# Performance work log

Measured on AMD Instinct MI355X. Metric: run time of the kernel, lower is better.

The kernel has to match this reference:

```python
import jax, jax.numpy as jnp
import numpy as np

U, P, D, H, E = 512, 1024, 128, 256, 98304
N = U + P


def setup_inputs() -> dict:
    key = jax.random.key(0)
    ks = jax.random.split(key, 16)
    def nrm(k, shape, scale=0.05):
        return jax.random.normal(k, shape, jnp.float32) * scale
    z = lambda *s: jnp.zeros(s, jnp.float32)
    return {
        "user_ids": jnp.arange(U),
        "paper_ids": jnp.arange(P),
        "edge_index": jax.random.randint(ks[0], (2, E), 0, N),
        "user_paper_interactions": jax.random.uniform(ks[1], (U, P), jnp.float32),
        "user_emb": nrm(ks[2], (U, D), 1.0),   # nn.Embedding tables
        "paper_emb": nrm(ks[3], (P, D), 1.0),
        "W0": nrm(ks[4], (D, H)), "b0": z(H),   # GCNConv weights (stored [in,out])
        "W1": nrm(ks[5], (H, H)), "b1": z(H),
        "W2": nrm(ks[6], (H, H)), "b2": z(H),
        "Wu": nrm(ks[7], (H, D)), "bu": z(D),   # user_output Linear
        "Wp": nrm(ks[8], (H, D)), "bp": z(D),   # paper_output Linear
        "Wq1": nrm(ks[9], (2 * D, H)), "bq1": z(H),  # predictor Linear 1
        "Wq2": nrm(ks[10], (H, 1)), "bq2": z(1),      # predictor Linear 2
    }


def gcn_conv(x, src, dst, W, b):
    """PyG GCNConv: add self-loops, symmetric D^-1/2 (A+I) D^-1/2 normalization."""
    n = x.shape[0]
    loop = jnp.arange(n)
    s = jnp.concatenate([src, loop])
    d = jnp.concatenate([dst, loop])
    deg = jax.ops.segment_sum(jnp.ones(d.shape, x.dtype), d, num_segments=n)
    dis = jnp.where(deg > 0, jax.lax.rsqrt(jnp.maximum(deg, 1.0)), 0.0)
    norm = dis[s] * dis[d]                      # [E+n]
    h = x @ W                                   # [n, H]
    out = jax.ops.segment_sum(h[s] * norm[:, None], d, num_segments=n)
    return out + b


def reference(user_ids, paper_ids, edge_index, user_paper_interactions,
              user_emb, paper_emb, W0, b0, W1, b1, W2, b2,
              Wu, bu, Wp, bp, Wq1, bq1, Wq2, bq2):
    # embedding lookups + node feature matrix [U+P, D]
    x = jnp.concatenate([user_emb[user_ids], paper_emb[paper_ids]], axis=0)
    src, dst = edge_index[0], edge_index[1]
    for W, b in ((W0, b0), (W1, b1), (W2, b2)):
        x = jax.nn.relu(gcn_conv(x, src, dst, W, b))  # dropout is identity in eval
    nu = user_ids.shape[0]
    np_ = paper_ids.shape[0]
    user_final = x[:nu] @ Wu + bu               # [U, D]
    paper_final = x[nu:] @ Wp + bp              # [P, D]
    # broadcast outer-product concat -> [U, P, 2D]
    combined = jnp.concatenate([
        jnp.broadcast_to(user_final[:, None, :], (nu, np_, user_final.shape[-1])),
        jnp.broadcast_to(paper_final[None, :, :], (nu, np_, paper_final.shape[-1])),
    ], axis=-1)
    h = jax.nn.relu(combined @ Wq1 + bq1)       # [U, P, H]
    pred = jax.nn.sigmoid(h @ Wq2 + bq2)[..., 0]  # [U, P]
    return pred
```

## Files before the change

### kernel.cpp

```cpp
#include <hip/hip_runtime.h>
#include <math.h>

constexpr int Uc = 512;
constexpr int Pc = 1024;
constexpr int Dc = 128;
constexpr int Hc = 256;
constexpr int Ec = 98304;
constexpr int Nc = 1536;
constexpr int CAP = 192;
constexpr int GRID = 768;
constexpr int BAR_STRIDE = 2304;

__device__ __forceinline__ void st_wt(float* p, float v) {
    __hip_atomic_store(p, v, __ATOMIC_RELAXED, __HIP_MEMORY_SCOPE_AGENT);
}
__device__ __forceinline__ void st_wt_i(int* p, int v) {
    __hip_atomic_store(p, v, __ATOMIC_RELAXED, __HIP_MEMORY_SCOPE_AGENT);
}
__device__ __forceinline__ void st_wt2(float* p, float2 v) {
    unsigned long long u;
    __builtin_memcpy(&u, &v, 8);
    __hip_atomic_store((unsigned long long*)p, u, __ATOMIC_RELAXED,
                       __HIP_MEMORY_SCOPE_AGENT);
}

__device__ __forceinline__ void gbar3(int* bb, int b) {
    __syncthreads();
    if (threadIdx.x == 0) {
        int leaf = b & 63;
        int lc = __hip_atomic_fetch_add(bb + leaf * 16, 1,
                                        __ATOMIC_RELAXED, __HIP_MEMORY_SCOPE_AGENT);
        if (lc == 11) {
            int mc = __hip_atomic_fetch_add(bb + 1024 + (leaf >> 3) * 16, 1,
                                            __ATOMIC_RELAXED, __HIP_MEMORY_SCOPE_AGENT);
            if (mc == 7) {
                int rc = __hip_atomic_fetch_add(bb + 1152, 1,
                                                __ATOMIC_RELAXED, __HIP_MEMORY_SCOPE_AGENT);
                if (rc == 7) {
#pragma unroll
                    for (int i = 0; i < 64; i++)
                        __hip_atomic_store(bb + 1216 + i * 16, 1, __ATOMIC_RELAXED,
                                           __HIP_MEMORY_SCOPE_AGENT);
                }
            }
        }
        int iters = 0;
        while (__hip_atomic_load(bb + 1216 + leaf * 16, __ATOMIC_RELAXED,
                                 __HIP_MEMORY_SCOPE_AGENT) == 0) {
            __builtin_amdgcn_s_sleep(8);
            if (++iters > (1 << 22)) break;
        }
    }
    __syncthreads();
}

__device__ __forceinline__ void fma4(float4& a, float n, const float4 r) {
    a.x += n * r.x; a.y += n * r.y; a.z += n * r.z; a.w += n * r.w;
}

union __align__(16) SharedU {
    struct {
        const float* sptr[2][CAP];
        float snrm[2][CAP];
        float pagg[4][Dc];
        float aggT[Dc][2];
        float red[4][2][Hc];
    } l0;
    struct {
        int sidx[2][CAP];
        float snrm[2][CAP];
        float pagg[4][Hc];
        float aggT[Hc][2];
        float xlocT[Hc][2];
        float red[4][2][Hc];
    } lh;
    struct {
        float auS[Hc * 8];
    } pr;
};

template <int K>
__device__ __forceinline__ void gemm_core16(const float* __restrict__ xr,
                                            const float* __restrict__ wc, int M,
                                            float& acc0, float& acc1) {
#pragma unroll 4
    for (int k = 0; k < K; k += 4) {
        float4 a = *(const float4*)(xr + k);
        float2 b0 = *(const float2*)(wc + (size_t)k * M);
        float2 b1 = *(const float2*)(wc + (size_t)(k + 1) * M);
        float2 b2 = *(const float2*)(wc + (size_t)(k + 2) * M);
        float2 b3 = *(const float2*)(wc + (size_t)(k + 3) * M);
        acc0 += a.x * b0.x; acc1 += a.x * b0.y;
        acc0 += a.y * b1.x; acc1 += a.y * b1.y;
        acc0 += a.z * b2.x; acc1 += a.z * b2.y;
        acc0 += a.w * b3.x; acc1 += a.w * b3.y;
    }
}

__device__ __forceinline__ void phase_front(
        int b, int t,
        const int* __restrict__ e_src, const int* __restrict__ e_dst,
        int* __restrict__ cnt, int* __restrict__ colF,
        const float* __restrict__ Wu, const float* __restrict__ Wp,
        const float* __restrict__ Wq1, const float* __restrict__ bu,
        const float* __restrict__ bp, const float* __restrict__ bq1,
        float* __restrict__ Wup, float* __restrict__ Wpp,
        float* __restrict__ bvu, float* __restrict__ bvp) {
    if (b < 384) {
        int e = b * 256 + t;
        int d = e_dst[e];
        int pos = atomicAdd(&cnt[d], 1);
        if (pos < CAP) st_wt_i(&colF[d * CAP + pos], e_src[e]);
    } else if (b < 640) {
        int id = b - 384;
        int z = id >> 7, tile = id & 127;
        int tx = t & 15, ty = t >> 4;
        const float* X = z ? Wp : Wu;
        const float* W = Wq1 + (z ? (size_t)Dc * Hc : 0);
        float* Y = z ? Wpp : Wup;
        int row = (tile >> 3) * 16 + ty, col = (tile & 7) * 32 + tx * 2;
        float a0 = 0.f, a1 = 0.f;
        gemm_core16<Dc>(X + (size_t)row * Dc, W + col, Hc, a0, a1);
        st_wt2(&Y[(size_t)row * Hc + col], make_float2(a0, a1));
    } else if (b == 640) {
        float s = bq1[t];
#pragma unroll 8
        for (int d = 0; d < Dc; d++) s += bu[d] * Wq1[d * Hc + t];
        st_wt(&bvu[t], s);
    } else if (b == 641) {
        float s = 0.f;
#pragma unroll 8
        for (int d = 0; d < Dc; d++) s += bp[d] * Wq1[(Dc + d) * Hc + t];
        st_wt(&bvp[t], s);
    }
}

__device__ void phase_l0(SharedU& su, int b, int t,
        const int* __restrict__ uid, const int* __restrict__ pid,
        const float* __restrict__ ue, const float* __restrict__ pe,
        const float* __restrict__ W0, const float* __restrict__ b0,
        const int* __restrict__ cnt, const int* __restrict__ colF,
        float* __restrict__ out) {
    int ibase = b * 2;
    int c[2]; float di[2];
#pragma unroll
    for (int r = 0; r < 2; r++) {
        c[r] = cnt[ibase + r];
        di[r] = rsqrtf((float)(c[r] + 1));
        int deg = min(c[r], CAP);
        if (t < deg) {
            int s = colF[(ibase + r) * CAP + t];
            su.l0.sptr[r][t] = (s < Uc) ? ue + (size_t)uid[s] * Dc
                                        : pe + (size_t)pid[s - Uc] * Dc;
            su.l0.snrm[r][t] = rsqrtf((float)(cnt[s] + 1));
        }
    }
    __syncthreads();
    {
        int wv = t >> 6, ln = t & 63;
        int r = wv >> 1, h = wv & 1;
        int i = ibase + r;
        int dg = min(c[r], CAP);
        int dg2 = dg >> 1;
        int j0 = h ? dg2 : 0, j1 = h ? dg : dg2;
        float2 acc = make_float2(0.f, 0.f);
        if (h == 0) {
            const float* xi = (i < Uc) ? ue + (size_t)uid[i] * Dc
                                       : pe + (size_t)pid[i - Uc] * Dc;
            float2 a2 = *(const float2*)(xi + ln * 2);
            acc.x = di[r] * a2.x;
            acc.y = di[r] * a2.y;
        }
        int j = j0;
        for (; j + 8 <= j1; j += 8) {
            float n0 = su.l0.snrm[r][j],     n1 = su.l0.snrm[r][j + 1];
            float n2 = su.l0.snrm[r][j + 2], n3 = su.l0.snrm[r][j + 3];
            float n4 = su.l0.snrm[r][j + 4], n5 = su.l0.snrm[r][j + 5];
            float n6 = su.l0.snrm[r][j + 6], n7 = su.l0.snrm[r][j + 7];
            float2 r0 = *(const float2*)(su.l0.sptr[r][j]     + ln * 2);
            float2 r1 = *(const float2*)(su.l0.sptr[r][j + 1] + ln * 2);
            float2 r2 = *(const float2*)(su.l0.sptr[r][j + 2] + ln * 2);
            float2 r3 = *(const float2*)(su.l0.sptr[r][j + 3] + ln * 2);
            float2 r4 = *(const float2*)(su.l0.sptr[r][j + 4] + ln * 2);
            float2 r5 = *(const float2*)(su.l0.sptr[r][j + 5] + ln * 2);
            float2 r6 = *(const float2*)(su.l0.sptr[r][j + 6] + ln * 2);
            float2 r7 = *(const float2*)(su.l0.sptr[r][j + 7] + ln * 2);
            acc.x += n0 * r0.x + n1 * r1.x + n2 * r2.x + n3 * r3.x;
            acc.y += n0 * r0.y + n1 * r1.y + n2 * r2.y + n3 * r3.y;
            acc.x += n4 * r4.x + n5 * r5.x + n6 * r6.x + n7 * r7.x;
            acc.y += n4 * r4.y + n5 * r5.y + n6 * r6.y + n7 * r7.y;
        }
        for (; j + 4 <= j1; j += 4) {
            float n0 = su.l0.snrm[r][j],     n1 = su.l0.snrm[r][j + 1];
            float n2 = su.l0.snrm[r][j + 2], n3 = su.l0.snrm[r][j + 3];
            float2 r0 = *(const float2*)(su.l0.sptr[r][j]     + ln * 2);
            float2 r1 = *(const float2*)(su.l0.sptr[r][j + 1] + ln * 2);
            float2 r2 = *(const float2*)(su.l0.sptr[r][j + 2] + ln * 2);
            float2 r3 = *(const float2*)(su.l0.sptr[r][j + 3] + ln * 2);
            acc.x += n0 * r0.x + n1 * r1.x + n2 * r2.x + n3 * r3.x;
            acc.y += n0 * r0.y + n1 * r1.y + n2 * r2.y + n3 * r3.y;
        }
        for (; j < j1; j++) {
            float2 r0 = *(const float2*)(su.l0.sptr[r][j] + ln * 2);
            acc.x += su.l0.snrm[r][j] * r0.x;
            acc.y += su.l0.snrm[r][j] * r0.y;
        }
        su.l0.pagg[wv][ln * 2]     = acc.x;
        su.l0.pagg[wv][ln * 2 + 1] = acc.y;
    }
    __syncthreads();
    {
        int r = t >> 7, f = t & 127;
        su.l0.aggT[f][r] = di[r] * (su.l0.pagg[2 * r][f] + su.l0.pagg[2 * r + 1][f]);
    }
    __syncthreads();
    {
        int wv = t >> 6, ln = t & 63;
        int k0 = wv * (Dc / 4);
        float4 a0 = {0.f, 0.f, 0.f, 0.f}, a1 = {0.f, 0.f, 0.f, 0.f};
        const float* Wp_ = W0 + (size_t)k0 * Hc + ln * 4;
#pragma unroll 8
        for (int kk = 0; kk < Dc / 4; kk++) {
            float2 g = *(const float2*)&su.l0.aggT[k0 + kk][0];
            float4 w = *(const float4*)(Wp_ + (size_t)kk * Hc);
            a0.x += g.x * w.x; a0.y += g.x * w.y; a0.z += g.x * w.z; a0.w += g.x * w.w;
            a1.x += g.y * w.x; a1.y += g.y * w.y; a1.z += g.y * w.z; a1.w += g.y * w.w;
        }
        *(float4*)&su.l0.red[wv][0][ln * 4] = a0;
        *(float4*)&su.l0.red[wv][1][ln * 4] = a1;
    }
    __syncthreads();
    {
        float bb = b0[t];
        float s0 = (su.l0.red[0][0][t] + su.l0.red[1][0][t]) +
                   (su.l0.red[2][0][t] + su.l0.red[3][0][t]) + bb;
        float s1 = (su.l0.red[0][1][t] + su.l0.red[1][1][t]) +
                   (su.l0.red[2][1][t] + su.l0.red[3][1][t]) + bb;
        st_wt(&out[(size_t)(ibase + 0) * Hc + t], fmaxf(s0, 0.f));
        st_wt(&out[(size_t)(ibase + 1) * Hc + t], fmaxf(s1, 0.f));
    }
}

__device__ __forceinline__ void agg_wave2(const float* __restrict__ X,
                                          const int (*sidx)[CAP], const float (*snrm)[CAP],
                                          const int* c, const float* di, int ibase,
                                          float (*pagg)[Hc], int t) {
    int wv = t >> 6, ln = t & 63;
    int r = wv >> 1, h = wv & 1;
    int dg = min(c[r], CAP);
    int dg2 = dg >> 1;
    int j0 = h ? dg2 : 0, j1 = h ? dg : dg2;
    float4 acc = make_float4(0.f, 0.f, 0.f, 0.f);
    if (h == 0) {
        acc = *(const float4*)&X[(size_t)(ibase + r) * Hc + ln * 4];
        acc.x *= di[r]; acc.y *= di[r]; acc.z *= di[r]; acc.w *= di[r];
    }
    int j = j0;
    for (; j + 8 <= j1; j += 8) {
        float n0 = snrm[r][j],     n1 = snrm[r][j + 1];
        float n2 = snrm[r][j + 2], n3 = snrm[r][j + 3];
        float n4 = snrm[r][j + 4], n5 = snrm[r][j + 5];
        float n6 = snrm[r][j + 6], n7 = snrm[r][j + 7];
        float4 r0 = *(const float4*)&X[sidx[r][j]     + ln * 4];
        float4 r1 = *(const float4*)&X[sidx[r][j + 1] + ln * 4];
        float4 r2 = *(const float4*)&X[sidx[r][j + 2] + ln * 4];
        float4 r3 = *(const float4*)&X[sidx[r][j + 3] + ln * 4];
        float4 r4 = *(const float4*)&X[sidx[r][j + 4] + ln * 4];
        float4 r5 = *(const float4*)&X[sidx[r][j + 5] + ln * 4];
        float4 r6 = *(const float4*)&X[sidx[r][j + 6] + ln * 4];
        float4 r7 = *(const float4*)&X[sidx[r][j + 7] + ln * 4];
        fma4(acc, n0, r0); fma4(acc, n1, r1); fma4(acc, n2, r2); fma4(acc, n3, r3);
        fma4(acc, n4, r4); fma4(acc, n5, r5); fma4(acc, n6, r6); fma4(acc, n7, r7);
    }
    for (; j + 4 <= j1; j += 4) {
        float n0 = snrm[r][j],     n1 = snrm[r][j + 1];
        float n2 = snrm[r][j + 2], n3 = snrm[r][j + 3];
        float4 r0 = *(const float4*)&X[sidx[r][j]     + ln * 4];
        float4 r1 = *(const float4*)&X[sidx[r][j + 1] + ln * 4];
        float4 r2 = *(const float4*)&X[sidx[r][j + 2] + ln * 4];
        float4 r3 = *(const float4*)&X[sidx[r][j + 3] + ln * 4];
        fma4(acc, n0, r0); fma4(acc, n1, r1); fma4(acc, n2, r2); fma4(acc, n3, r3);
    }
    for (; j < j1; j++) {
        float4 r0 = *(const float4*)&X[sidx[r][j] + ln * 4];
        fma4(acc, snrm[r][j], r0);
    }
    *(float4*)&pagg[wv][ln * 4] = acc;
}

__device__ __forceinline__ void gemv_wsplit(const float (*aggT)[2],
                                            const float* __restrict__ W,
                                            float (*red)[2][Hc], int t) {
    int wv = t >> 6, ln = t & 63;
    int k0 = wv * (Hc / 4);
    float4 a0 = {0.f, 0.f, 0.f, 0.f}, a1 = {0.f, 0.f, 0.f, 0.f};
    const float* Wp_ = W + (size_t)k0 * Hc + ln * 4;
#pragma unroll 8
    for (int kk = 0; kk < Hc / 4; kk++) {
        float2 g = *(const float2*)&aggT[k0 + kk][0];
        float4 w = *(const float4*)(Wp_ + (size_t)kk * Hc);
        a0.x += g.x * w.x; a0.y += g.x * w.y; a0.z += g.x * w.z; a0.w += g.x * w.w;
        a1.x += g.y * w.x; a1.y += g.y * w.y; a1.z += g.y * w.z; a1.w += g.y * w.w;
    }
    *(float4*)&red[wv][0][ln * 4] = a0;
    *(float4*)&red[wv][1][ln * 4] = a1;
}

__device__ __forceinline__ void layer_head(SharedU& su, int b, int t,
        const float* __restrict__ X, const int* __restrict__ cnt,
        const int* __restrict__ colF, int* c, float* di) {
    int ibase = b * 2;
#pragma unroll
    for (int r = 0; r < 2; r++) {
        c[r] = cnt[ibase + r];
        di[r] = rsqrtf((float)(c[r] + 1));
        int deg = min(c[r], CAP);
        if (t < deg) {
            int s = colF[(ibase + r) * CAP + t];
            su.lh.sidx[r][t] = s * Hc;
            su.lh.snrm[r][t] = rsqrtf((float)(cnt[s] + 1));
        }
    }
    __syncthreads();
    agg_wave2(X, su.lh.sidx, su.lh.snrm, c, di, ibase, su.lh.pagg, t);
    __syncthreads();
    *(float2*)&su.lh.aggT[t][0] =
        make_float2(di[0] * (su.lh.pagg[0][t] + su.lh.pagg[1][t]),
                    di[1] * (su.lh.pagg[2][t] + su.lh.pagg[3][t]));
    __syncthreads();
}

__device__ void phase_lh(SharedU& su, int b, int t,
        const float* __restrict__ X, const float* __restrict__ W,
        const float* __restrict__ bias, const int* __restrict__ cnt,
        const int* __restrict__ colF, float* __restrict__ out) {
    int c[2]; float di[2];
    layer_head(su, b, t, X, cnt, colF, c, di);
    gemv_wsplit(su.lh.aggT, W, su.lh.red, t);
    __syncthreads();
    int ibase = b * 2;
    float bb = bias[t];
    float s0 = (su.lh.red[0][0][t] + su.lh.red[1][0][t]) +
               (su.lh.red[2][0][t] + su.lh.red[3][0][t]) + bb;
    float s1 = (su.lh.red[0][1][t] + su.lh.red[1][1][t]) +
               (su.lh.red[2][1][t] + su.lh.red[3][1][t]) + bb;
    st_wt(&out[(size_t)(ibase + 0) * Hc + t], fmaxf(s0, 0.f));
    st_wt(&out[(size_t)(ibase + 1) * Hc + t], fmaxf(s1, 0.f));
}

__device__ void phase_lht(SharedU& su, int b, int t,
        const float* __restrict__ X, const float* __restrict__ W2,
        const float* __restrict__ b2, const int* __restrict__ cnt,
        const int* __restrict__ colF,
        const float* __restrict__ Wup, const float* __restrict__ Wpp,
        const float* __restrict__ bvu, const float* __restrict__ bvp,
        float* __restrict__ AuT, float* __restrict__ ApT) {
    int c[2]; float di[2];
    layer_head(su, b, t, X, cnt, colF, c, di);
    gemv_wsplit(su.lh.aggT, W2, su.lh.red, t);
    __syncthreads();
    {
        float bb = b2[t];
        float s0 = (su.lh.red[0][0][t] + su.lh.red[1][0][t]) +
                   (su.lh.red[2][0][t] + su.lh.red[3][0][t]) + bb;
        float s1 = (su.lh.red[0][1][t] + su.lh.red[1][1][t]) +
                   (su.lh.red[2][1][t] + su.lh.red[3][1][t]) + bb;
        *(float2*)&su.lh.xlocT[t][0] = make_float2(fmaxf(s0, 0.f), fmaxf(s1, 0.f));
    }
    __syncthreads();
    gemv_wsplit(su.lh.xlocT, (b < 256) ? Wup : Wpp, su.lh.red, t);
    __syncthreads();
    {
        int ibase = b * 2;
        const float* bsel = (b < 256) ? bvu : bvp;
        float* YT  = (b < 256) ? AuT : ApT;
        int ldy    = (b < 256) ? Uc : Pc;
        int rloc   = (b < 256) ? ibase : ibase - Uc;
        float bb = bsel[t];
        float s0 = (su.lh.red[0][0][t] + su.lh.red[1][0][t]) +
                   (su.lh.red[2][0][t] + su.lh.red[3][0][t]) + bb;
        float s1 = (su.lh.red[0][1][t] + su.lh.red[1][1][t]) +
                   (su.lh.red[2][1][t] + su.lh.red[3][1][t]) + bb;
        st_wt2(&YT[(size_t)t * ldy + rloc], make_float2(s0, s1));
    }
}

__device__ void phase_pred(float* auS, int b, int t,
        const float* __restrict__ AuT, const float* __restrict__ ApT,
        const float* __restrict__ Wq2, const float* __restrict__ bq2,
        float* __restrict__ out) {
    int ub = (b >> 3) * 8, pb = (b & 7) * 128;
#pragma unroll
    for (int i = t; i < Hc * 8; i += 256) {
        int k = i >> 3, u = i & 7;
        auS[i] = AuT[(size_t)k * Uc + ub + u];
    }
    __syncthreads();
    int wv = t >> 6, ln = t & 63;
    const float* app = ApT + pb + ln * 2;
    const float* aup = auS + wv * 2;
    float acc[2][2] = {};
#pragma unroll 4
    for (int k = 0; k < Hc; k++) {
        float w = Wq2[k];
        float2 a = *(const float2*)(aup + k * 8);
        float2 p = *(const float2*)(app + (size_t)k * Pc);
        acc[0][0] += fmaxf(a.x + p.x, 0.f) * w;
        acc[0][1] += fmaxf(a.x + p.y, 0.f) * w;
        acc[1][0] += fmaxf(a.y + p.x, 0.f) * w;
        acc[1][1] += fmaxf(a.y + p.y, 0.f) * w;
    }
    float bq = bq2[0];
#pragma unroll
    for (int r = 0; r < 2; r++) {
        int u = ub + wv * 2 + r;
        float2 o;
        o.x = 1.f / (1.f + __expf(-(acc[r][0] + bq)));
        o.y = 1.f / (1.f + __expf(-(acc[r][1] + bq)));
        *(float2*)&out[(size_t)u * Pc + pb + ln * 2] = o;
    }
}

struct KArgs {
    const int *uid, *pid, *e_src, *e_dst;
    const float *ue, *pe;
    const float *W0, *b0, *W1, *b1, *W2, *b2;
    const float *Wu, *bu, *Wp, *bp, *Wq1, *bq1, *Wq2, *bq2;
    int *cnt, *colF, *bar;
    float *xA, *xB, *Wup, *Wpp, *bvu, *bvp, *AuT, *ApT, *pred;
};

__global__ void __launch_bounds__(256) k_all(KArgs A) {
    __shared__ SharedU su;
    int t = threadIdx.x, b = blockIdx.x;
    phase_front(b, t, A.e_src, A.e_dst, A.cnt, A.colF, A.Wu, A.Wp, A.Wq1,
                A.bu, A.bp, A.bq1, A.Wup, A.Wpp, A.bvu, A.bvp);
    gbar3(A.bar + 0 * BAR_STRIDE, b);
    phase_l0(su, b, t, A.uid, A.pid, A.ue, A.pe, A.W0, A.b0, A.cnt, A.colF, A.xA);
    gbar3(A.bar + 1 * BAR_STRIDE, b);
    phase_lh(su, b, t, A.xA, A.W1, A.b1, A.cnt, A.colF, A.xB);
    gbar3(A.bar + 2 * BAR_STRIDE, b);
    phase_lht(su, b, t, A.xB, A.W2, A.b2, A.cnt, A.colF,
              A.Wup, A.Wpp, A.bvu, A.bvp, A.AuT, A.ApT);
    gbar3(A.bar + 3 * BAR_STRIDE, b);
    if (b < 512) phase_pred(su.pr.auS, b, t, A.AuT, A.ApT, A.Wq2, A.bq2, A.pred);
}

extern "C" void kernel_launch(void* const* d_in, const int* in_sizes, int n_in,
                              void* d_out, int out_size, void* d_ws, size_t ws_size,
                              hipStream_t stream) {
    KArgs A;
    A.uid = (const int*)d_in[0];
    A.pid = (const int*)d_in[1];
    const int* ei = (const int*)d_in[2];
    A.e_src = ei;
    A.e_dst = ei + Ec;
    A.ue  = (const float*)d_in[4];
    A.pe  = (const float*)d_in[5];
    A.W0  = (const float*)d_in[6];  A.b0  = (const float*)d_in[7];
    A.W1  = (const float*)d_in[8];  A.b1  = (const float*)d_in[9];
    A.W2  = (const float*)d_in[10]; A.b2  = (const float*)d_in[11];
    A.Wu  = (const float*)d_in[12]; A.bu  = (const float*)d_in[13];
    A.Wp  = (const float*)d_in[14]; A.bp  = (const float*)d_in[15];
    A.Wq1 = (const float*)d_in[16]; A.bq1 = (const float*)d_in[17];
    A.Wq2 = (const float*)d_in[18]; A.bq2 = (const float*)d_in[19];

    char* w = (char*)d_ws;
    auto alloc = [&](size_t bytes) { char* p = w; w += (bytes + 255) & ~size_t(255); return p; };
    constexpr int BAR_BYTES = 4 * BAR_STRIDE * 4;
    int* zreg = (int*)alloc(Nc * 4 + BAR_BYTES);
    A.cnt  = zreg;
    A.bar  = zreg + Nc;
    A.colF = (int*)alloc((size_t)Nc * CAP * 4);
    A.xA   = (float*)alloc((size_t)Nc * Hc * 4);
    A.xB   = (float*)alloc((size_t)Nc * Hc * 4);
    A.Wup  = (float*)alloc((size_t)Hc * Hc * 4);
    A.Wpp  = (float*)alloc((size_t)Hc * Hc * 4);
    A.bvu  = (float*)alloc(Hc * 4);
    A.bvp  = (float*)alloc(Hc * 4);
    A.AuT  = (float*)alloc((size_t)Hc * Uc * 4);
    A.ApT  = (float*)alloc((size_t)Hc * Pc * 4);
    A.pred = (float*)d_out;

    hipMemsetAsync(A.cnt, 0, Nc * 4 + BAR_BYTES, stream);
    k_all<<<GRID, 256, 0, stream>>>(A);
}
```

Measured before the change: 193.9 us.

## Replace grid barriers between GCN layers with per-block dataflow flags

```diff
diff --git a/kernel.cpp b/kernel.cpp
--- a/kernel.cpp
+++ b/kernel.cpp
@@ -9,6 +9,7 @@
 constexpr int Nc = 1536;
 constexpr int CAP = 192;
 constexpr int GRID = 768;
+constexpr int CSTR = 16;
 constexpr int BAR_STRIDE = 2304;
 
 __device__ __forceinline__ void st_wt(float* p, float v) {
@@ -22,6 +23,15 @@
     __builtin_memcpy(&u, &v, 8);
     __hip_atomic_store((unsigned long long*)p, u, __ATOMIC_RELAXED,
                        __HIP_MEMORY_SCOPE_AGENT);
+}
+
+__device__ __forceinline__ void wait_ep(const int* ep, int blk) {
+    int it = 0;
+    while (__hip_atomic_load(ep + blk, __ATOMIC_RELAXED,
+                             __HIP_MEMORY_SCOPE_AGENT) == 0) {
+        __builtin_amdgcn_s_sleep(4);
+        if (++it > (1 << 22)) break;
+    }
 }
 
 __device__ __forceinline__ void gbar3(int* bb, int b) {
@@ -109,7 +119,7 @@
     if (b < 384) {
         int e = b * 256 + t;
         int d = e_dst[e];
-        int pos = atomicAdd(&cnt[d], 1);
+        int pos = atomicAdd(&cnt[d * CSTR], 1);
         if (pos < CAP) st_wt_i(&colF[d * CAP + pos], e_src[e]);
     } else if (b < 640) {
         int id = b - 384;
@@ -140,19 +150,19 @@
         const float* __restrict__ ue, const float* __restrict__ pe,
         const float* __restrict__ W0, const float* __restrict__ b0,
         const int* __restrict__ cnt, const int* __restrict__ colF,
-        float* __restrict__ out) {
+        float* __restrict__ out, int* __restrict__ ep1) {
     int ibase = b * 2;
     int c[2]; float di[2];
 #pragma unroll
     for (int r = 0; r < 2; r++) {
-        c[r] = cnt[ibase + r];
+        c[r] = cnt[(ibase + r) * CSTR];
         di[r] = rsqrtf((float)(c[r] + 1));
         int deg = min(c[r], CAP);
         if (t < deg) {
             int s = colF[(ibase + r) * CAP + t];
             su.l0.sptr[r][t] = (s < Uc) ? ue + (size_t)uid[s] * Dc
                                         : pe + (size_t)pid[s - Uc] * Dc;
-            su.l0.snrm[r][t] = rsqrtf((float)(cnt[s] + 1));
+            su.l0.snrm[r][t] = rsqrtf((float)(cnt[s * CSTR] + 1));
         }
     }
     __syncthreads();
@@ -239,6 +249,8 @@
         st_wt(&out[(size_t)(ibase + 0) * Hc + t], fmaxf(s0, 0.f));
         st_wt(&out[(size_t)(ibase + 1) * Hc + t], fmaxf(s1, 0.f));
     }
+    __syncthreads();
+    if (t == 0) st_wt_i(&ep1[b], 1);
 }
 
 __device__ __forceinline__ void agg_wave2(const float* __restrict__ X,
@@ -308,17 +320,19 @@
 
 __device__ __forceinline__ void layer_head(SharedU& su, int b, int t,
         const float* __restrict__ X, const int* __restrict__ cnt,
-        const int* __restrict__ colF, int* c, float* di) {
+        const int* __restrict__ colF, const int* __restrict__ ep_in,
+        int* c, float* di) {
     int ibase = b * 2;
 #pragma unroll
     for (int r = 0; r < 2; r++) {
-        c[r] = cnt[ibase + r];
+        c[r] = cnt[(ibase + r) * CSTR];
         di[r] = rsqrtf((float)(c[r] + 1));
         int deg = min(c[r], CAP);
         if (t < deg) {
             int s = colF[(ibase + r) * CAP + t];
+            wait_ep(ep_in, s >> 1);
             su.lh.sidx[r][t] = s * Hc;
-            su.lh.snrm[r][t] = rsqrtf((float)(cnt[s] + 1));
+            su.lh.snrm[r][t] = rsqrtf((float)(cnt[s * CSTR] + 1));
         }
     }
     __syncthreads();
@@ -333,9 +347,10 @@
 __device__ void phase_lh(SharedU& su, int b, int t,
         const float* __restrict__ X, const float* __restrict__ W,
         const float* __restrict__ bias, const int* __restrict__ cnt,
-        const int* __restrict__ colF, float* __restrict__ out) {
+        const int* __restrict__ colF, const int* __restrict__ ep_in,
+        float* __restrict__ out, int* __restrict__ ep_out) {
     int c[2]; float di[2];
-    layer_head(su, b, t, X, cnt, colF, c, di);
+    layer_head(su, b, t, X, cnt, colF, ep_in, c, di);
     gemv_wsplit(su.lh.aggT, W, su.lh.red, t);
     __syncthreads();
     int ibase = b * 2;
@@ -346,17 +361,20 @@
                (su.lh.red[2][1][t] + su.lh.red[3][1][t]) + bb;
     st_wt(&out[(size_t)(ibase + 0) * Hc + t], fmaxf(s0, 0.f));
     st_wt(&out[(size_t)(ibase + 1) * Hc + t], fmaxf(s1, 0.f));
+    __syncthreads();
+    if (t == 0) st_wt_i(&ep_out[b], 1);
 }
 
 __device__ void phase_lht(SharedU& su, int b, int t,
         const float* __restrict__ X, const float* __restrict__ W2,
         const float* __restrict__ b2, const int* __restrict__ cnt,
-        const int* __restrict__ colF,
+        const int* __restrict__ colF, const int* __restrict__ ep_in,
         const float* __restrict__ Wup, const float* __restrict__ Wpp,
         const float* __restrict__ bvu, const float* __restrict__ bvp,
-        float* __restrict__ AuT, float* __restrict__ ApT) {
+        float* __restrict__ AuT, float* __restrict__ ApT,
+        int* __restrict__ ep_out) {
     int c[2]; float di[2];
-    layer_head(su, b, t, X, cnt, colF, c, di);
+    layer_head(su, b, t, X, cnt, colF, ep_in, c, di);
     gemv_wsplit(su.lh.aggT, W2, su.lh.red, t);
     __syncthreads();
     {
@@ -383,13 +401,21 @@
                    (su.lh.red[2][1][t] + su.lh.red[3][1][t]) + bb;
         st_wt2(&YT[(size_t)t * ldy + rloc], make_float2(s0, s1));
     }
+    __syncthreads();
+    if (t == 0) st_wt_i(&ep_out[b], 1);
 }
 
 __device__ void phase_pred(float* auS, int b, int t,
         const float* __restrict__ AuT, const float* __restrict__ ApT,
         const float* __restrict__ Wq2, const float* __restrict__ bq2,
-        float* __restrict__ out) {
+        const int* __restrict__ ep3, float* __restrict__ out) {
     int ub = (b >> 3) * 8, pb = (b & 7) * 128;
+    if (t < 68) {
+        int blk = (t < 4) ? (ub >> 1) + t
+                          : 256 + (pb >> 1) + (t - 4);
+        wait_ep(ep3, blk);
+    }
+    __syncthreads();
 #pragma unroll
     for (int i = t; i < Hc * 8; i += 256) {
         int k = i >> 3, u = i & 7;
@@ -426,7 +452,7 @@
     const float *ue, *pe;
     const float *W0, *b0, *W1, *b1, *W2, *b2;
     const float *Wu, *bu, *Wp, *bp, *Wq1, *bq1, *Wq2, *bq2;
-    int *cnt, *colF, *bar;
+    int *cnt, *colF, *bar, *ep1, *ep2, *ep3;
     float *xA, *xB, *Wup, *Wpp, *bvu, *bvp, *AuT, *ApT, *pred;
 };
 
@@ -435,15 +461,14 @@
     int t = threadIdx.x, b = blockIdx.x;
     phase_front(b, t, A.e_src, A.e_dst, A.cnt, A.colF, A.Wu, A.Wp, A.Wq1,
                 A.bu, A.bp, A.bq1, A.Wup, A.Wpp, A.bvu, A.bvp);
-    gbar3(A.bar + 0 * BAR_STRIDE, b);
-    phase_l0(su, b, t, A.uid, A.pid, A.ue, A.pe, A.W0, A.b0, A.cnt, A.colF, A.xA);
-    gbar3(A.bar + 1 * BAR_STRIDE, b);
-    phase_lh(su, b, t, A.xA, A.W1, A.b1, A.cnt, A.colF, A.xB);
-    gbar3(A.bar + 2 * BAR_STRIDE, b);
-    phase_lht(su, b, t, A.xB, A.W2, A.b2, A.cnt, A.colF,
-              A.Wup, A.Wpp, A.bvu, A.bvp, A.AuT, A.ApT);
-    gbar3(A.bar + 3 * BAR_STRIDE, b);
-    if (b < 512) phase_pred(su.pr.auS, b, t, A.AuT, A.ApT, A.Wq2, A.bq2, A.pred);
+    gbar3(A.bar, b);
+    phase_l0(su, b, t, A.uid, A.pid, A.ue, A.pe, A.W0, A.b0, A.cnt, A.colF,
+             A.xA, A.ep1);
+    phase_lh(su, b, t, A.xA, A.W1, A.b1, A.cnt, A.colF, A.ep1, A.xB, A.ep2);
+    phase_lht(su, b, t, A.xB, A.W2, A.b2, A.cnt, A.colF, A.ep2,
+              A.Wup, A.Wpp, A.bvu, A.bvp, A.AuT, A.ApT, A.ep3);
+    if (b < 512) phase_pred(su.pr.auS, b, t, A.AuT, A.ApT, A.Wq2, A.bq2,
+                            A.ep3, A.pred);
 }
 
 extern "C" void kernel_launch(void* const* d_in, const int* in_sizes, int n_in,
@@ -467,21 +492,28 @@
 
     char* w = (char*)d_ws;
     auto alloc = [&](size_t bytes) { char* p = w; w += (bytes + 255) & ~size_t(255); return p; };
-    constexpr int BAR_BYTES = 4 * BAR_STRIDE * 4;
-    int* zreg = (int*)alloc(Nc * 4 + BAR_BYTES);
+    constexpr int ZINTS = Nc * CSTR + BAR_STRIDE + 3 * GRID;
+    int* zreg = (int*)alloc((size_t)ZINTS * 4);
     A.cnt  = zreg;
-    A.bar  = zreg + Nc;
+    A.bar  = zreg + Nc * CSTR;
+    A.ep1  = A.bar + BAR_STRIDE;
+    A.ep2  = A.ep1 + GRID;
+    A.ep3  = A.ep2 + GRID;
     A.colF = (int*)alloc((size_t)Nc * CAP * 4);
+    alloc(4096);
     A.xA   = (float*)alloc((size_t)Nc * Hc * 4);
+    alloc(4096);
     A.xB   = (float*)alloc((size_t)Nc * Hc * 4);
+    alloc(4096);
     A.Wup  = (float*)alloc((size_t)Hc * Hc * 4);
     A.Wpp  = (float*)alloc((size_t)Hc * Hc * 4);
     A.bvu  = (float*)alloc(Hc * 4);
     A.bvp  = (float*)alloc(Hc * 4);
+    alloc(4096);
     A.AuT  = (float*)alloc((size_t)Hc * Uc * 4);
     A.ApT  = (float*)alloc((size_t)Hc * Pc * 4);
     A.pred = (float*)d_out;
 
-    hipMemsetAsync(A.cnt, 0, Nc * 4 + BAR_BYTES, stream);
+    hipMemsetAsync(zreg, 0, (size_t)ZINTS * 4, stream);
     k_all<<<GRID, 256, 0, stream>>>(A);
 }
```

After: 204.9 us. 5.6% more time.

## Replace final grid barrier with per-block readiness flags and cache edge norms

Applied to the files above, without the earlier changes.

```diff
diff --git a/kernel.cpp b/kernel.cpp
--- a/kernel.cpp
+++ b/kernel.cpp
@@ -52,6 +52,15 @@
         }
     }
     __syncthreads();
+}
+
+__device__ __forceinline__ void wait_ep(const int* ep, int blk) {
+    int it = 0;
+    while (__hip_atomic_load(ep + blk, __ATOMIC_RELAXED,
+                             __HIP_MEMORY_SCOPE_AGENT) == 0) {
+        __builtin_amdgcn_s_sleep(16);
+        if (++it > (1 << 21)) break;
+    }
 }
 
 __device__ __forceinline__ void fma4(float4& a, float n, const float4 r) {
@@ -140,7 +149,7 @@
         const float* __restrict__ ue, const float* __restrict__ pe,
         const float* __restrict__ W0, const float* __restrict__ b0,
         const int* __restrict__ cnt, const int* __restrict__ colF,
-        float* __restrict__ out) {
+        float* __restrict__ nrmF, float* __restrict__ out) {
     int ibase = b * 2;
     int c[2]; float di[2];
 #pragma unroll
@@ -152,7 +161,9 @@
             int s = colF[(ibase + r) * CAP + t];
             su.l0.sptr[r][t] = (s < Uc) ? ue + (size_t)uid[s] * Dc
                                         : pe + (size_t)pid[s - Uc] * Dc;
-            su.l0.snrm[r][t] = rsqrtf((float)(cnt[s] + 1));
+            float nv = rsqrtf((float)(cnt[s] + 1));
+            su.l0.snrm[r][t] = nv;
+            st_wt(&nrmF[(size_t)(ibase + r) * CAP + t], nv);
         }
     }
     __syncthreads();
@@ -308,7 +319,8 @@
 
 __device__ __forceinline__ void layer_head(SharedU& su, int b, int t,
         const float* __restrict__ X, const int* __restrict__ cnt,
-        const int* __restrict__ colF, int* c, float* di) {
+        const int* __restrict__ colF, const float* __restrict__ nrmF,
+        int* c, float* di) {
     int ibase = b * 2;
 #pragma unroll
     for (int r = 0; r < 2; r++) {
@@ -318,7 +330,7 @@
         if (t < deg) {
             int s = colF[(ibase + r) * CAP + t];
             su.lh.sidx[r][t] = s * Hc;
-            su.lh.snrm[r][t] = rsqrtf((float)(cnt[s] + 1));
+            su.lh.snrm[r][t] = nrmF[(size_t)(ibase + r) * CAP + t];
         }
     }
     __syncthreads();
@@ -333,9 +345,10 @@
 __device__ void phase_lh(SharedU& su, int b, int t,
         const float* __restrict__ X, const float* __restrict__ W,
         const float* __restrict__ bias, const int* __restrict__ cnt,
-        const int* __restrict__ colF, float* __restrict__ out) {
+        const int* __restrict__ colF, const float* __restrict__ nrmF,
+        float* __restrict__ out) {
     int c[2]; float di[2];
-    layer_head(su, b, t, X, cnt, colF, c, di);
+    layer_head(su, b, t, X, cnt, colF, nrmF, c, di);
     gemv_wsplit(su.lh.aggT, W, su.lh.red, t);
     __syncthreads();
     int ibase = b * 2;
@@ -351,12 +364,13 @@
 __device__ void phase_lht(SharedU& su, int b, int t,
         const float* __restrict__ X, const float* __restrict__ W2,
         const float* __restrict__ b2, const int* __restrict__ cnt,
-        const int* __restrict__ colF,
+        const int* __restrict__ colF, const float* __restrict__ nrmF,
         const float* __restrict__ Wup, const float* __restrict__ Wpp,
         const float* __restrict__ bvu, const float* __restrict__ bvp,
-        float* __restrict__ AuT, float* __restrict__ ApT) {
+        float* __restrict__ AuT, float* __restrict__ ApT,
+        int* __restrict__ ep3) {
     int c[2]; float di[2];
-    layer_head(su, b, t, X, cnt, colF, c, di);
+    layer_head(su, b, t, X, cnt, colF, nrmF, c, di);
     gemv_wsplit(su.lh.aggT, W2, su.lh.red, t);
     __syncthreads();
     {
@@ -383,42 +397,48 @@
                    (su.lh.red[2][1][t] + su.lh.red[3][1][t]) + bb;
         st_wt2(&YT[(size_t)t * ldy + rloc], make_float2(s0, s1));
     }
+    __syncthreads();
+    if (t == 0) st_wt_i(&ep3[b], 1);
 }
 
 __device__ void phase_pred(float* auS, int b, int t,
         const float* __restrict__ AuT, const float* __restrict__ ApT,
         const float* __restrict__ Wq2, const float* __restrict__ bq2,
-        float* __restrict__ out) {
-    int ub = (b >> 3) * 8, pb = (b & 7) * 128;
+        const int* __restrict__ ep3, float* __restrict__ out) {
+    int ub = (b >> 2) * 4, pb = (b & 3) * 256;
+    if (t < 130) {
+        int blk = (t < 2) ? (ub >> 1) + t
+                          : 256 + (pb >> 1) + (t - 2);
+        wait_ep(ep3, blk);
+    }
+    __syncthreads();
 #pragma unroll
-    for (int i = t; i < Hc * 8; i += 256) {
-        int k = i >> 3, u = i & 7;
+    for (int i = t; i < Hc * 4; i += 256) {
+        int k = i >> 2, u = i & 3;
         auS[i] = AuT[(size_t)k * Uc + ub + u];
     }
     __syncthreads();
     int wv = t >> 6, ln = t & 63;
-    const float* app = ApT + pb + ln * 2;
-    const float* aup = auS + wv * 2;
-    float acc[2][2] = {};
+    const float* app = ApT + pb + ln * 4;
+    const float* aup = auS + wv;
+    float4 acc = {0.f, 0.f, 0.f, 0.f};
 #pragma unroll 4
     for (int k = 0; k < Hc; k++) {
         float w = Wq2[k];
-        float2 a = *(const float2*)(aup + k * 8);
-        float2 p = *(const float2*)(app + (size_t)k * Pc);
-        acc[0][0] += fmaxf(a.x + p.x, 0.f) * w;
-        acc[0][1] += fmaxf(a.x + p.y, 0.f) * w;
-        acc[1][0] += fmaxf(a.y + p.x, 0.f) * w;
-        acc[1][1] += fmaxf(a.y + p.y, 0.f) * w;
+        float a = aup[k * 4];
+        float4 p = *(const float4*)(app + (size_t)k * Pc);
+        acc.x += fmaxf(a + p.x, 0.f) * w;
+        acc.y += fmaxf(a + p.y, 0.f) * w;
+        acc.z += fmaxf(a + p.z, 0.f) * w;
+        acc.w += fmaxf(a + p.w, 0.f) * w;
     }
     float bq = bq2[0];
-#pragma unroll
-    for (int r = 0; r < 2; r++) {
-        int u = ub + wv * 2 + r;
-        float2 o;
-        o.x = 1.f / (1.f + __expf(-(acc[r][0] + bq)));
-        o.y = 1.f / (1.f + __expf(-(acc[r][1] + bq)));
-        *(float2*)&out[(size_t)u * Pc + pb + ln * 2] = o;
-    }
+    float4 o;
+    o.x = 1.f / (1.f + __expf(-(acc.x + bq)));
+    o.y = 1.f / (1.f + __expf(-(acc.y + bq)));
+    o.z = 1.f / (1.f + __expf(-(acc.z + bq)));
+    o.w = 1.f / (1.f + __expf(-(acc.w + bq)));
+    *(float4*)&out[(size_t)(ub + wv) * Pc + pb + ln * 4] = o;
 }
 
 struct KArgs {
@@ -426,8 +446,8 @@
     const float *ue, *pe;
     const float *W0, *b0, *W1, *b1, *W2, *b2;
     const float *Wu, *bu, *Wp, *bp, *Wq1, *bq1, *Wq2, *bq2;
-    int *cnt, *colF, *bar;
-    float *xA, *xB, *Wup, *Wpp, *bvu, *bvp, *AuT, *ApT, *pred;
+    int *cnt, *colF, *bar, *ep3;
+    float *nrmF, *xA, *xB, *Wup, *Wpp, *bvu, *bvp, *AuT, *ApT, *pred;
 };
 
 __global__ void __launch_bounds__(256) k_all(KArgs A) {
@@ -436,14 +456,15 @@
     phase_front(b, t, A.e_src, A.e_dst, A.cnt, A.colF, A.Wu, A.Wp, A.Wq1,
                 A.bu, A.bp, A.bq1, A.Wup, A.Wpp, A.bvu, A.bvp);
     gbar3(A.bar + 0 * BAR_STRIDE, b);
-    phase_l0(su, b, t, A.uid, A.pid, A.ue, A.pe, A.W0, A.b0, A.cnt, A.colF, A.xA);
+    phase_l0(su, b, t, A.uid, A.pid, A.ue, A.pe, A.W0, A.b0, A.cnt, A.colF,
+             A.nrmF, A.xA);
     gbar3(A.bar + 1 * BAR_STRIDE, b);
-    phase_lh(su, b, t, A.xA, A.W1, A.b1, A.cnt, A.colF, A.xB);
+    phase_lh(su, b, t, A.xA, A.W1, A.b1, A.cnt, A.colF, A.nrmF, A.xB);
     gbar3(A.bar + 2 * BAR_STRIDE, b);
-    phase_lht(su, b, t, A.xB, A.W2, A.b2, A.cnt, A.colF,
-              A.Wup, A.Wpp, A.bvu, A.bvp, A.AuT, A.ApT);
-    gbar3(A.bar + 3 * BAR_STRIDE, b);
-    if (b < 512) phase_pred(su.pr.auS, b, t, A.AuT, A.ApT, A.Wq2, A.bq2, A.pred);
+    phase_lht(su, b, t, A.xB, A.W2, A.b2, A.cnt, A.colF, A.nrmF,
+              A.Wup, A.Wpp, A.bvu, A.bvp, A.AuT, A.ApT, A.ep3);
+    if (b < 512) phase_pred(su.pr.auS, b, t, A.AuT, A.ApT, A.Wq2, A.bq2,
+                            A.ep3, A.pred);
 }
 
 extern "C" void kernel_launch(void* const* d_in, const int* in_sizes, int n_in,
@@ -467,11 +488,13 @@
 
     char* w = (char*)d_ws;
     auto alloc = [&](size_t bytes) { char* p = w; w += (bytes + 255) & ~size_t(255); return p; };
-    constexpr int BAR_BYTES = 4 * BAR_STRIDE * 4;
-    int* zreg = (int*)alloc(Nc * 4 + BAR_BYTES);
+    constexpr int ZINTS = Nc + 3 * BAR_STRIDE + GRID;
+    int* zreg = (int*)alloc((size_t)ZINTS * 4);
     A.cnt  = zreg;
     A.bar  = zreg + Nc;
+    A.ep3  = A.bar + 3 * BAR_STRIDE;
     A.colF = (int*)alloc((size_t)Nc * CAP * 4);
+    A.nrmF = (float*)alloc((size_t)Nc * CAP * 4);
     A.xA   = (float*)alloc((size_t)Nc * Hc * 4);
     A.xB   = (float*)alloc((size_t)Nc * Hc * 4);
     A.Wup  = (float*)alloc((size_t)Hc * Hc * 4);
@@ -482,6 +505,6 @@
     A.ApT  = (float*)alloc((size_t)Hc * Pc * 4);
     A.pred = (float*)d_out;
 
-    hipMemsetAsync(A.cnt, 0, Nc * 4 + BAR_BYTES, stream);
+    hipMemsetAsync(zreg, 0, (size_t)ZINTS * 4, stream);
     k_all<<<GRID, 256, 0, stream>>>(A);
 }
```

Result: slower. 200.9 us (+3.6%).

## Replace final grid barrier with per-block ready flags and use 16-bit adjacency

Applied to the files above, without the earlier changes.

```diff
diff --git a/kernel.cpp b/kernel.cpp
--- a/kernel.cpp
+++ b/kernel.cpp
@@ -15,6 +15,9 @@
     __hip_atomic_store(p, v, __ATOMIC_RELAXED, __HIP_MEMORY_SCOPE_AGENT);
 }
 __device__ __forceinline__ void st_wt_i(int* p, int v) {
+    __hip_atomic_store(p, v, __ATOMIC_RELAXED, __HIP_MEMORY_SCOPE_AGENT);
+}
+__device__ __forceinline__ void st_wt_u16(unsigned short* p, unsigned short v) {
     __hip_atomic_store(p, v, __ATOMIC_RELAXED, __HIP_MEMORY_SCOPE_AGENT);
 }
 __device__ __forceinline__ void st_wt2(float* p, float2 v) {
@@ -52,6 +55,15 @@
         }
     }
     __syncthreads();
+}
+
+__device__ __forceinline__ void wait_ep(const int* ep, int blk) {
+    int it = 0;
+    while (__hip_atomic_load(ep + blk, __ATOMIC_RELAXED,
+                             __HIP_MEMORY_SCOPE_AGENT) == 0) {
+        __builtin_amdgcn_s_sleep(16);
+        if (++it > (1 << 21)) break;
+    }
 }
 
 __device__ __forceinline__ void fma4(float4& a, float n, const float4 r) {
@@ -100,7 +112,7 @@
 __device__ __forceinline__ void phase_front(
         int b, int t,
         const int* __restrict__ e_src, const int* __restrict__ e_dst,
-        int* __restrict__ cnt, int* __restrict__ colF,
+        int* __restrict__ cnt, unsigned short* __restrict__ colF,
         const float* __restrict__ Wu, const float* __restrict__ Wp,
         const float* __restrict__ Wq1, const float* __restrict__ bu,
         const float* __restrict__ bp, const float* __restrict__ bq1,
@@ -110,7 +122,7 @@
         int e = b * 256 + t;
         int d = e_dst[e];
         int pos = atomicAdd(&cnt[d], 1);
-        if (pos < CAP) st_wt_i(&colF[d * CAP + pos], e_src[e]);
+        if (pos < CAP) st_wt_u16(&colF[d * CAP + pos], (unsigned short)e_src[e]);
     } else if (b < 640) {
         int id = b - 384;
         int z = id >> 7, tile = id & 127;
@@ -139,7 +151,7 @@
         const int* __restrict__ uid, const int* __restrict__ pid,
         const float* __restrict__ ue, const float* __restrict__ pe,
         const float* __restrict__ W0, const float* __restrict__ b0,
-        const int* __restrict__ cnt, const int* __restrict__ colF,
+        const int* __restrict__ cnt, const unsigned short* __restrict__ colF,
         float* __restrict__ out) {
     int ibase = b * 2;
     int c[2]; float di[2];
@@ -308,7 +320,8 @@
 
 __device__ __forceinline__ void layer_head(SharedU& su, int b, int t,
         const float* __restrict__ X, const int* __restrict__ cnt,
-        const int* __restrict__ colF, int* c, float* di) {
+        const unsigned short* __restrict__ colF,
+        int* c, float* di) {
     int ibase = b * 2;
 #pragma unroll
     for (int r = 0; r < 2; r++) {
@@ -333,7 +346,7 @@
 __device__ void phase_lh(SharedU& su, int b, int t,
         const float* __restrict__ X, const float* __restrict__ W,
         const float* __restrict__ bias, const int* __restrict__ cnt,
-        const int* __restrict__ colF, float* __restrict__ out) {
+        const unsigned short* __restrict__ colF, float* __restrict__ out) {
     int c[2]; float di[2];
     layer_head(su, b, t, X, cnt, colF, c, di);
     gemv_wsplit(su.lh.aggT, W, su.lh.red, t);
@@ -351,10 +364,11 @@
 __device__ void phase_lht(SharedU& su, int b, int t,
         const float* __restrict__ X, const float* __restrict__ W2,
         const float* __restrict__ b2, const int* __restrict__ cnt,
-        const int* __restrict__ colF,
+        const unsigned short* __restrict__ colF,
         const float* __restrict__ Wup, const float* __restrict__ Wpp,
         const float* __restrict__ bvu, const float* __restrict__ bvp,
-        float* __restrict__ AuT, float* __restrict__ ApT) {
+        float* __restrict__ AuT, float* __restrict__ ApT,
+        int* __restrict__ ep3) {
     int c[2]; float di[2];
     layer_head(su, b, t, X, cnt, colF, c, di);
     gemv_wsplit(su.lh.aggT, W2, su.lh.red, t);
@@ -383,13 +397,21 @@
                    (su.lh.red[2][1][t] + su.lh.red[3][1][t]) + bb;
         st_wt2(&YT[(size_t)t * ldy + rloc], make_float2(s0, s1));
     }
+    __syncthreads();
+    if (t == 0) st_wt_i(&ep3[b], 1);
 }
 
 __device__ void phase_pred(float* auS, int b, int t,
         const float* __restrict__ AuT, const float* __restrict__ ApT,
         const float* __restrict__ Wq2, const float* __restrict__ bq2,
-        float* __restrict__ out) {
+        const int* __restrict__ ep3, float* __restrict__ out) {
     int ub = (b >> 3) * 8, pb = (b & 7) * 128;
+    if (t < 68) {
+        int blk = (t < 4) ? (ub >> 1) + t
+                          : 256 + (pb >> 1) + (t - 4);
+        wait_ep(ep3, blk);
+    }
+    __syncthreads();
 #pragma unroll
     for (int i = t; i < Hc * 8; i += 256) {
         int k = i >> 3, u = i & 7;
@@ -426,7 +448,8 @@
     const float *ue, *pe;
     const float *W0, *b0, *W1, *b1, *W2, *b2;
     const float *Wu, *bu, *Wp, *bp, *Wq1, *bq1, *Wq2, *bq2;
-    int *cnt, *colF, *bar;
+    int *cnt, *bar, *ep3;
+    unsigned short *colF;
     float *xA, *xB, *Wup, *Wpp, *bvu, *bvp, *AuT, *ApT, *pred;
 };
 
@@ -441,9 +464,9 @@
     phase_lh(su, b, t, A.xA, A.W1, A.b1, A.cnt, A.colF, A.xB);
     gbar3(A.bar + 2 * BAR_STRIDE, b);
     phase_lht(su, b, t, A.xB, A.W2, A.b2, A.cnt, A.colF,
-              A.Wup, A.Wpp, A.bvu, A.bvp, A.AuT, A.ApT);
-    gbar3(A.bar + 3 * BAR_STRIDE, b);
-    if (b < 512) phase_pred(su.pr.auS, b, t, A.AuT, A.ApT, A.Wq2, A.bq2, A.pred);
+              A.Wup, A.Wpp, A.bvu, A.bvp, A.AuT, A.ApT, A.ep3);
+    if (b < 512) phase_pred(su.pr.auS, b, t, A.AuT, A.ApT, A.Wq2, A.bq2,
+                            A.ep3, A.pred);
 }
 
 extern "C" void kernel_launch(void* const* d_in, const int* in_sizes, int n_in,
@@ -467,11 +490,12 @@
 
     char* w = (char*)d_ws;
     auto alloc = [&](size_t bytes) { char* p = w; w += (bytes + 255) & ~size_t(255); return p; };
-    constexpr int BAR_BYTES = 4 * BAR_STRIDE * 4;
-    int* zreg = (int*)alloc(Nc * 4 + BAR_BYTES);
+    constexpr int ZINTS = Nc + 3 * BAR_STRIDE + GRID;
+    int* zreg = (int*)alloc((size_t)ZINTS * 4);
     A.cnt  = zreg;
     A.bar  = zreg + Nc;
-    A.colF = (int*)alloc((size_t)Nc * CAP * 4);
+    A.ep3  = A.bar + 3 * BAR_STRIDE;
+    A.colF = (unsigned short*)alloc((size_t)Nc * CAP * 2);
     A.xA   = (float*)alloc((size_t)Nc * Hc * 4);
     A.xB   = (float*)alloc((size_t)Nc * Hc * 4);
     A.Wup  = (float*)alloc((size_t)Hc * Hc * 4);
@@ -482,6 +506,6 @@
     A.ApT  = (float*)alloc((size_t)Hc * Pc * 4);
     A.pred = (float*)d_out;
 
-    hipMemsetAsync(A.cnt, 0, Nc * 4 + BAR_BYTES, stream);
+    hipMemsetAsync(zreg, 0, (size_t)ZINTS * 4, stream);
     k_all<<<GRID, 256, 0, stream>>>(A);
 }
```

New measurement: 198.7 us. 1.02x slower.
